# Optimization experiments

Hardware: AMD Instinct MI355X
Metric: run time of the kernel (lower is better)

## Reference

```python
import jax, jax.numpy as jnp
import numpy as np

VOCAB = 32000
EMBED = 512
NUM_CLASS = 5
LEAVES = 8192
N_NODES = 2 * LEAVES - 1


def _build_tree(n_leaves):
    """Balanced binary tree over n_leaves leaves, nodes listed in post-order
    (children always appear before their parent), matching the recursive
    traversal order of the original torch module."""
    is_leaf, word, left, right = [], [], [], []

    def rec(lo, hi):
        if hi - lo == 1:
            is_leaf.append(1)
            word.append((lo * 2654435761) % VOCAB)
            left.append(0)
            right.append(0)
        else:
            mid = (lo + hi) // 2
            l = rec(lo, mid)
            r = rec(mid, hi)
            is_leaf.append(0)
            word.append(0)
            left.append(l)
            right.append(r)
        return len(is_leaf) - 1

    rec(0, n_leaves)
    return (np.asarray(is_leaf, np.int32), np.asarray(word, np.int32),
            np.asarray(left, np.int32), np.asarray(right, np.int32))


def setup_inputs() -> dict:
    key = jax.random.key(0)
    k1, k2, k3, k4, k5 = jax.random.split(key, 5)
    is_leaf, word, left, right = _build_tree(LEAVES)
    scale = 0.05
    return {
        "is_leaf": jnp.asarray(is_leaf),
        "word": jnp.asarray(word),
        "left": jnp.asarray(left),
        "right": jnp.asarray(right),
        "emb": jax.random.normal(k1, (VOCAB, EMBED), jnp.float32) * scale,
        "W": jax.random.normal(k2, (EMBED, 2 * EMBED), jnp.float32) * scale,
        "bW": jax.random.normal(k3, (EMBED,), jnp.float32) * scale,
        "P": jax.random.normal(k4, (NUM_CLASS, EMBED), jnp.float32) * scale,
        "bP": jax.random.normal(k5, (NUM_CLASS,), jnp.float32) * scale,
    }


def reference(is_leaf, word, left, right, emb, W, bW, P, bP):
    n = is_leaf.shape[0]

    def step(H, xs):
        idx, lf, wd, li, ri = xs
        # internal node: relu(W @ [h_left; h_right] + b)
        pair = jnp.concatenate([H[li], H[ri]])          # [2D]
        internal = pair @ W.T + bW                       # [D]
        leaf = emb[wd]                                   # [D]
        h = jax.nn.relu(jnp.where(lf == 1, leaf, internal))
        return H.at[idx].set(h), None

    H0 = jnp.zeros((n, EMBED), emb.dtype)
    xs = (jnp.arange(n, dtype=jnp.int32), is_leaf, word, left, right)
    H, _ = jax.lax.scan(step, H0, xs)
    # per-node class logits, rows in traversal (post-)order: [N, num_class]
    return H @ P.T + bP
```

## Files before the change

### kernel.cpp

```cpp
#include <hip/hip_runtime.h>


#define EMBED 512
#define K2    1024
#define WOFF  (EMBED * K2)

typedef _Float16 half8 __attribute__((ext_vector_type(8)));
typedef _Float16 half4 __attribute__((ext_vector_type(4)));
typedef float    floatx4 __attribute__((ext_vector_type(4)));

__device__ __forceinline__ float relu_f(float x) { return fmaxf(x, 0.0f); }

__global__ __launch_bounds__(256)
void packleaf(const float* __restrict__ W, const float* __restrict__ emb,
              const int* __restrict__ word,
              _Float16* __restrict__ Whp,
              _Float16* __restrict__ Hh, _Float16* __restrict__ Hl,
              int nLeaves)
{
    int tid = threadIdx.x;
    int wave = tid >> 6, lane = tid & 63;

    {
        int t = blockIdx.x * 256 + tid;
        int n = t >> 7, kc = t & 127;
        const float* src = W + (size_t)n * K2 + kc * 8;
        int s = kc >> 2, quad = kc & 3;
        int ln = (quad << 4) | (n & 15);
        size_t off = (size_t)(n >> 4) * 16384 + (size_t)s * 512 + (size_t)ln * 8;
        half8 hi, lo;
#pragma unroll
        for (int j = 0; j < 8; ++j) {
            float w = src[j];
            _Float16 h16 = (_Float16)w;
            hi[j] = h16;
            lo[j] = (_Float16)(w - (float)h16);
        }
        *(half8*)(Whp + off) = hi;
        *(half8*)(Whp + WOFF + off) = lo;
    }
    {
#pragma unroll
        for (int i = 0; i < 8; ++i) {
            int m = blockIdx.x * 32 + wave * 8 + i;
            if (m < nLeaves) {
                int idx = 2 * m - __popc(m);
                int wd = word[idx];
                const float4* src = (const float4*)(emb + (size_t)wd * EMBED) + lane * 2;
                float4 a = src[0], b = src[1];
                float v[8] = {a.x, a.y, a.z, a.w, b.x, b.y, b.z, b.w};
                half8 hi, lo;
#pragma unroll
                for (int j = 0; j < 8; ++j) {
                    float x = relu_f(v[j]);
                    _Float16 h16 = (_Float16)x;
                    hi[j] = h16;
                    lo[j] = (_Float16)(x - (float)h16);
                }
                *(half8*)(Hh + (size_t)idx * EMBED + lane * 8) = hi;
                *(half8*)(Hl + (size_t)idx * EMBED + lane * 8) = lo;
            }
        }
    }
}

__global__ __launch_bounds__(256)
void gemm_splitk32(const _Float16* __restrict__ Hh, const _Float16* __restrict__ Hl,
                   const _Float16* __restrict__ Wp,
                   const float* __restrict__ bW,
                   _Float16* HhO, _Float16* HlO,
                   int h, int M)
{
    __shared__ float red[4096];

    int tid = threadIdx.x;
    int wave = tid >> 6, lane = tid & 63;
    int q = lane >> 4, r = lane & 15;
    int m0 = blockIdx.x * 32, n0 = blockIdx.y * 32;

    const _Float16 *pAh[2], *pAl[2];
#pragma unroll
    for (int mi = 0; mi < 2; ++mi) {
        int m = m0 + mi * 16 + r;
        int idx = ((m + 1) << (h + 1)) - 2 - __popc(m);
        int childRow = (wave < 2) ? (idx - (1 << h)) : (idx - 1);
        int kbase = (wave & 1) * 256;
        pAh[mi] = Hh + (size_t)childRow * EMBED + kbase + q * 8;
        pAl[mi] = Hl + (size_t)childRow * EMBED + kbase + q * 8;
    }
    const _Float16* pB[2];
#pragma unroll
    for (int ui = 0; ui < 2; ++ui)
        pB[ui] = Wp + (size_t)(blockIdx.y * 2 + ui) * 16384
               + (size_t)(wave * 8) * 512 + lane * 8;

    floatx4 acc[2][2];
#pragma unroll
    for (int mi = 0; mi < 2; ++mi)
#pragma unroll
        for (int ui = 0; ui < 2; ++ui) acc[mi][ui] = (floatx4){0.f, 0.f, 0.f, 0.f};

#pragma unroll
    for (int s = 0; s < 8; ++s) {
        half8 ah[2], al[2], bh[2], bl[2];
#pragma unroll
        for (int mi = 0; mi < 2; ++mi) {
            ah[mi] = *(const half8*)(pAh[mi] + s * 32);
            al[mi] = *(const half8*)(pAl[mi] + s * 32);
        }
#pragma unroll
        for (int ui = 0; ui < 2; ++ui) {
            bh[ui] = *(const half8*)(pB[ui] + s * 512);
            bl[ui] = *(const half8*)(pB[ui] + s * 512 + WOFF);
        }
#pragma unroll
        for (int mi = 0; mi < 2; ++mi)
#pragma unroll
            for (int ui = 0; ui < 2; ++ui) {
                acc[mi][ui] = __builtin_amdgcn_mfma_f32_16x16x32_f16(ah[mi], bh[ui], acc[mi][ui], 0, 0, 0);
                acc[mi][ui] = __builtin_amdgcn_mfma_f32_16x16x32_f16(ah[mi], bl[ui], acc[mi][ui], 0, 0, 0);
                acc[mi][ui] = __builtin_amdgcn_mfma_f32_16x16x32_f16(al[mi], bh[ui], acc[mi][ui], 0, 0, 0);
            }
    }

#pragma unroll
    for (int mi = 0; mi < 2; ++mi)
#pragma unroll
        for (int ui = 0; ui < 2; ++ui)
#pragma unroll
            for (int reg = 0; reg < 4; ++reg)
                red[wave * 1024 + (mi * 16 + q * 4 + reg) * 32 + ui * 16 + r]
                    = acc[mi][ui][reg];
    __syncthreads();

    int row = tid >> 3, c4 = (tid & 7) * 4;
    int mm = m0 + row;
    int node = ((mm + 1) << (h + 1)) - 2 - __popc(mm);
    half4 hi4, lo4;
#pragma unroll
    for (int j = 0; j < 4; ++j) {
        int c = row * 32 + c4 + j;
        float v = red[c] + red[1024 + c] + red[2048 + c] + red[3072 + c];
        float x = relu_f(v + bW[n0 + c4 + j]);
        _Float16 hi = (_Float16)x;
        hi4[j] = hi;
        lo4[j] = (_Float16)(x - (float)hi);
    }
    *(half4*)(HhO + (size_t)node * EMBED + n0 + c4) = hi4;
    *(half4*)(HlO + (size_t)node * EMBED + n0 + c4) = lo4;
}

__global__ __launch_bounds__(256)
void gemm_splitk(const _Float16* __restrict__ Hh, const _Float16* __restrict__ Hl,
                 const _Float16* __restrict__ Wp,
                 const float* __restrict__ bW,
                 _Float16* HhO, _Float16* HlO,
                 int h, int M)
{
    __shared__ float red[4 * 256];

    int tid = threadIdx.x;
    int wave = tid >> 6, lane = tid & 63;
    int q = lane >> 4, r = lane & 15;
    int mt = blockIdx.x, u = blockIdx.y;

    int m = mt * 16 + r;
    if (m >= M) m = M - 1;
    int idx = ((m + 1) << (h + 1)) - 2 - __popc(m);
    int childRow = (wave < 2) ? (idx - (1 << h)) : (idx - 1);
    int kbase = (wave & 1) * 256;
    const _Float16* pAh = Hh + (size_t)childRow * EMBED + kbase + q * 8;
    const _Float16* pAl = Hl + (size_t)childRow * EMBED + kbase + q * 8;
    const _Float16* pB  = Wp + (size_t)u * 16384 + (size_t)(wave * 8) * 512 + lane * 8;

    floatx4 acc = (floatx4){0.f, 0.f, 0.f, 0.f};
#pragma unroll
    for (int s = 0; s < 8; ++s) {
        half8 ah = *(const half8*)(pAh + s * 32);
        half8 al = *(const half8*)(pAl + s * 32);
        half8 bh = *(const half8*)(pB + s * 512);
        half8 bl = *(const half8*)(pB + s * 512 + WOFF);
        acc = __builtin_amdgcn_mfma_f32_16x16x32_f16(ah, bh, acc, 0, 0, 0);
        acc = __builtin_amdgcn_mfma_f32_16x16x32_f16(ah, bl, acc, 0, 0, 0);
        acc = __builtin_amdgcn_mfma_f32_16x16x32_f16(al, bh, acc, 0, 0, 0);
    }
#pragma unroll
    for (int reg = 0; reg < 4; ++reg)
        red[wave * 256 + (q * 4 + reg) * 16 + r] = acc[reg];
    __syncthreads();

    int row = tid >> 4, col = tid & 15;
    float v = red[row * 16 + col] + red[256 + row * 16 + col]
            + red[512 + row * 16 + col] + red[768 + row * 16 + col];
    int mm = mt * 16 + row;
    if (mm < M) {
        int node = ((mm + 1) << (h + 1)) - 2 - __popc(mm);
        int colg = u * 16 + col;
        float x = relu_f(v + bW[colg]);
        _Float16 hi = (_Float16)x;
        HhO[(size_t)node * EMBED + colg] = hi;
        HlO[(size_t)node * EMBED + colg] = (_Float16)(x - (float)hi);
    }
}

__global__ __launch_bounds__(256)
void out_kernel(const _Float16* __restrict__ Hh, const _Float16* __restrict__ Hl,
                const float* __restrict__ P, const float* __restrict__ bP,
                float* __restrict__ out, int nNodes)
{
    int t = blockIdx.x * 256 + threadIdx.x;
    int node = t >> 6, lane = t & 63;
    if (node >= nNodes) return;
    half8 hv = *(const half8*)(Hh + (size_t)node * EMBED + lane * 8);
    half8 lv = *(const half8*)(Hl + (size_t)node * EMBED + lane * 8);
    float hx[8];
#pragma unroll
    for (int j = 0; j < 8; ++j) hx[j] = (float)hv[j] + (float)lv[j];
    float s[5];
#pragma unroll
    for (int c = 0; c < 5; ++c) {
        const float* p = P + c * EMBED + lane * 8;
        float4 p0 = *(const float4*)p;
        float4 p1 = *(const float4*)(p + 4);
        s[c] = hx[0] * p0.x + hx[1] * p0.y + hx[2] * p0.z + hx[3] * p0.w
             + hx[4] * p1.x + hx[5] * p1.y + hx[6] * p1.z + hx[7] * p1.w;
    }
#pragma unroll
    for (int o = 32; o > 0; o >>= 1)
#pragma unroll
        for (int c = 0; c < 5; ++c)
            s[c] += __shfl_down(s[c], o, 64);
    if (lane == 0) {
#pragma unroll
        for (int c = 0; c < 5; ++c)
            out[(size_t)node * 5 + c] = s[c] + bP[c];
    }
}

extern "C" void kernel_launch(void* const* d_in, const int* in_sizes, int n_in,
                              void* d_out, int out_size, void* d_ws, size_t ws_size,
                              hipStream_t stream)
{
    const int*   word = (const int*)d_in[1];
    const float* emb  = (const float*)d_in[4];
    const float* W    = (const float*)d_in[5];
    const float* bW   = (const float*)d_in[6];
    const float* P    = (const float*)d_in[7];
    const float* bP   = (const float*)d_in[8];
    float* out = (float*)d_out;

    int nNodes  = in_sizes[0];
    int nLeaves = (nNodes + 1) / 2;

    int hoff = (nNodes + 1) * EMBED;
    _Float16* Hh  = (_Float16*)d_ws;
    _Float16* Hl  = Hh + hoff;
    _Float16* Whp = Hl + hoff;

    packleaf<<<dim3(256), dim3(256), 0, stream>>>(
        W, emb, word, Whp, Hh, Hl, nLeaves);
    for (int h = 1; h <= 4; ++h) {
        int M = 1 << (13 - h);
        gemm_splitk32<<<dim3(M / 32, 16), dim3(256), 0, stream>>>(
            Hh, Hl, Whp, bW, Hh, Hl, h, M);
    }
    for (int h = 5; h <= 13; ++h) {
        int M = 1 << (13 - h);
        gemm_splitk<<<dim3((M + 15) / 16, 32), dim3(256), 0, stream>>>(
            Hh, Hl, Whp, bW, Hh, Hl, h, M);
    }
    out_kernel<<<dim3((nNodes * 64 + 255) / 256), dim3(256), 0, stream>>>(
        Hh, Hl, P, bP, out, nNodes);
}
```

Baseline: 252.8 us.

## Store hidden states level-contiguous and add LDS-staged 64x64 GEMM for bottom levels

Hidden-state rows are now laid out level by level (leaves first, then each tree level contiguously), so the two children of node m sit at adjacent rows 2m and 2m+1. Row indexing in the GEMMs becomes a plain offset, and only the output kernel maps back to post-order. The two largest levels get a new 64x64-tile kernel that stages A through LDS with global_load_lds and reduces a 2-way K split in shared memory, to improve reuse and coalescing over the old 32x32 split-K kernel. The cost is a more complex kernel with extra barriers per K chunk, and stores to C that are now scalar and strided.

```diff
diff --git a/kernel.cpp b/kernel.cpp
--- a/kernel.cpp
+++ b/kernel.cpp
@@ -6,10 +6,16 @@
 #define WOFF  (EMBED * K2)
 
 typedef _Float16 half8 __attribute__((ext_vector_type(8)));
-typedef _Float16 half4 __attribute__((ext_vector_type(4)));
 typedef float    floatx4 __attribute__((ext_vector_type(4)));
 
 __device__ __forceinline__ float relu_f(float x) { return fmaxf(x, 0.0f); }
+
+#define GLDS16(gp, lp)                                                        \
+    __builtin_amdgcn_global_load_lds(                                         \
+        (const __attribute__((address_space(1))) void*)(gp),                  \
+        (__attribute__((address_space(3))) void*)(lp), 16, 0, 0)
+
+#define MFMA16(a, b, c) __builtin_amdgcn_mfma_f32_16x16x32_f16(a, b, c, 0, 0, 0)
 
 __global__ __launch_bounds__(256)
 void packleaf(const float* __restrict__ W, const float* __restrict__ emb,
@@ -44,8 +50,7 @@
         for (int i = 0; i < 8; ++i) {
             int m = blockIdx.x * 32 + wave * 8 + i;
             if (m < nLeaves) {
-                int idx = 2 * m - __popc(m);
-                int wd = word[idx];
+                int wd = word[2 * m - __popc(m)];
                 const float4* src = (const float4*)(emb + (size_t)wd * EMBED) + lane * 2;
                 float4 a = src[0], b = src[1];
                 float v[8] = {a.x, a.y, a.z, a.w, b.x, b.y, b.z, b.w};
@@ -57,19 +62,110 @@
                     hi[j] = h16;
                     lo[j] = (_Float16)(x - (float)h16);
                 }
-                *(half8*)(Hh + (size_t)idx * EMBED + lane * 8) = hi;
-                *(half8*)(Hl + (size_t)idx * EMBED + lane * 8) = lo;
-            }
-        }
-    }
-}
-
-__global__ __launch_bounds__(256)
-void gemm_splitk32(const _Float16* __restrict__ Hh, const _Float16* __restrict__ Hl,
-                   const _Float16* __restrict__ Wp,
+                *(half8*)(Hh + (size_t)m * EMBED + lane * 8) = hi;
+                *(half8*)(Hl + (size_t)m * EMBED + lane * 8) = lo;
+            }
+        }
+    }
+}
+
+__global__ __launch_bounds__(256)
+void gemm_lvl(const _Float16* __restrict__ Ap,
+              const _Float16* __restrict__ Wp,
+              const float* __restrict__ bW,
+              _Float16* __restrict__ Cp,
+              int hoff)
+{
+    __shared__ _Float16 As[16384];
+    __shared__ float Red[4096];
+
+    int tid = threadIdx.x;
+    int wave = tid >> 6, lane = tid & 63;
+    int q = lane >> 4, r = lane & 15;
+    int slice = wave >> 1, nh = wave & 1;
+    int bm0 = blockIdx.x * 64, bn0 = blockIdx.y * 64;
+
+    const _Float16* Asrc = Ap + (size_t)(nh ? hoff : 0)
+                         + (size_t)(bm0 + r) * 1024 + slice * 512 + q * 8;
+
+    floatx4 acc[4][2];
+#pragma unroll
+    for (int t = 0; t < 4; ++t)
+#pragma unroll
+        for (int u = 0; u < 2; ++u) acc[t][u] = (floatx4){0.f, 0.f, 0.f, 0.f};
+
+    for (int kc = 0; kc < 8; ++kc) {
+#pragma unroll
+        for (int t = 0; t < 4; ++t)
+#pragma unroll
+            for (int s2 = 0; s2 < 2; ++s2) {
+                const _Float16* gp = Asrc + t * (16 * 1024) + kc * 64 + s2 * 32;
+                GLDS16(gp, &As[(slice * 16 + t * 4 + s2 * 2 + nh) * 512]);
+            }
+        __syncthreads();
+
+#pragma unroll
+        for (int s2 = 0; s2 < 2; ++s2) {
+            half8 bh[2], bl[2];
+#pragma unroll
+            for (int u = 0; u < 2; ++u) {
+                const _Float16* pb = Wp + (size_t)(blockIdx.y * 4 + nh * 2 + u) * 16384
+                                   + (size_t)(slice * 16 + kc * 2 + s2) * 512 + lane * 8;
+                bh[u] = *(const half8*)pb;
+                bl[u] = *(const half8*)(pb + WOFF);
+            }
+#pragma unroll
+            for (int t = 0; t < 4; ++t) {
+                half8 ah = *(const half8*)&As[(slice * 16 + t * 4 + s2 * 2 + 0) * 512 + lane * 8];
+                half8 al = *(const half8*)&As[(slice * 16 + t * 4 + s2 * 2 + 1) * 512 + lane * 8];
+#pragma unroll
+                for (int u = 0; u < 2; ++u) {
+                    acc[t][u] = MFMA16(ah, bh[u], acc[t][u]);
+                    acc[t][u] = MFMA16(ah, bl[u], acc[t][u]);
+                    acc[t][u] = MFMA16(al, bh[u], acc[t][u]);
+                }
+            }
+        }
+        __syncthreads();
+    }
+
+    if (slice == 1) {
+#pragma unroll
+        for (int t = 0; t < 4; ++t)
+#pragma unroll
+            for (int u = 0; u < 2; ++u)
+#pragma unroll
+                for (int reg = 0; reg < 4; ++reg)
+                    Red[(t * 16 + q * 4 + reg) * 64 + nh * 32 + u * 16 + r]
+                        = acc[t][u][reg];
+    }
+    __syncthreads();
+    if (slice == 0) {
+#pragma unroll
+        for (int t = 0; t < 4; ++t)
+#pragma unroll
+            for (int u = 0; u < 2; ++u) {
+                int col = bn0 + nh * 32 + u * 16 + r;
+                float bw = bW[col];
+#pragma unroll
+                for (int reg = 0; reg < 4; ++reg) {
+                    int ml = t * 16 + q * 4 + reg;
+                    float v = acc[t][u][reg]
+                            + Red[ml * 64 + nh * 32 + u * 16 + r];
+                    float x = relu_f(v + bw);
+                    _Float16 hi = (_Float16)x;
+                    size_t o = (size_t)(bm0 + ml) * EMBED + col;
+                    Cp[o] = hi;
+                    Cp[o + hoff] = (_Float16)(x - (float)hi);
+                }
+            }
+    }
+}
+
+__global__ __launch_bounds__(256)
+void gemm_splitk32(const _Float16* __restrict__ Ap, const _Float16* __restrict__ Wp,
                    const float* __restrict__ bW,
-                   _Float16* HhO, _Float16* HlO,
-                   int h, int M)
+                   _Float16* __restrict__ Cp, int hoff)
 {
     __shared__ float red[4096];
 
@@ -82,23 +178,22 @@
 #pragma unroll
     for (int mi = 0; mi < 2; ++mi) {
         int m = m0 + mi * 16 + r;
-        int idx = ((m + 1) << (h + 1)) - 2 - __popc(m);
-        int childRow = (wave < 2) ? (idx - (1 << h)) : (idx - 1);
-        int kbase = (wave & 1) * 256;
-        pAh[mi] = Hh + (size_t)childRow * EMBED + kbase + q * 8;
-        pAl[mi] = Hl + (size_t)childRow * EMBED + kbase + q * 8;
+        int prow = 2 * m + (wave >> 1);
+        int kb = (wave & 1) * 256;
+        pAh[mi] = Ap + (size_t)prow * EMBED + kb + q * 8;
+        pAl[mi] = pAh[mi] + hoff;
     }
     const _Float16* pB[2];
 #pragma unroll
-    for (int ui = 0; ui < 2; ++ui)
-        pB[ui] = Wp + (size_t)(blockIdx.y * 2 + ui) * 16384
-               + (size_t)(wave * 8) * 512 + lane * 8;
+    for (int u = 0; u < 2; ++u)
+        pB[u] = Wp + (size_t)(blockIdx.y * 2 + u) * 16384
+              + (size_t)(wave * 8) * 512 + lane * 8;
 
     floatx4 acc[2][2];
 #pragma unroll
     for (int mi = 0; mi < 2; ++mi)
 #pragma unroll
-        for (int ui = 0; ui < 2; ++ui) acc[mi][ui] = (floatx4){0.f, 0.f, 0.f, 0.f};
+        for (int u = 0; u < 2; ++u) acc[mi][u] = (floatx4){0.f, 0.f, 0.f, 0.f};
 
 #pragma unroll
     for (int s = 0; s < 8; ++s) {
@@ -109,34 +204,32 @@
             al[mi] = *(const half8*)(pAl[mi] + s * 32);
         }
 #pragma unroll
-        for (int ui = 0; ui < 2; ++ui) {
-            bh[ui] = *(const half8*)(pB[ui] + s * 512);
-            bl[ui] = *(const half8*)(pB[ui] + s * 512 + WOFF);
+        for (int u = 0; u < 2; ++u) {
+            bh[u] = *(const half8*)(pB[u] + s * 512);
+            bl[u] = *(const half8*)(pB[u] + s * 512 + WOFF);
         }
 #pragma unroll
         for (int mi = 0; mi < 2; ++mi)
 #pragma unroll
-            for (int ui = 0; ui < 2; ++ui) {
-                acc[mi][ui] = __builtin_amdgcn_mfma_f32_16x16x32_f16(ah[mi], bh[ui], acc[mi][ui], 0, 0, 0);
-                acc[mi][ui] = __builtin_amdgcn_mfma_f32_16x16x32_f16(ah[mi], bl[ui], acc[mi][ui], 0, 0, 0);
-                acc[mi][ui] = __builtin_amdgcn_mfma_f32_16x16x32_f16(al[mi], bh[ui], acc[mi][ui], 0, 0, 0);
+            for (int u = 0; u < 2; ++u) {
+                acc[mi][u] = MFMA16(ah[mi], bh[u], acc[mi][u]);
+                acc[mi][u] = MFMA16(ah[mi], bl[u], acc[mi][u]);
+                acc[mi][u] = MFMA16(al[mi], bh[u], acc[mi][u]);
             }
     }
 
 #pragma unroll
     for (int mi = 0; mi < 2; ++mi)
 #pragma unroll
-        for (int ui = 0; ui < 2; ++ui)
+        for (int u = 0; u < 2; ++u)
 #pragma unroll
             for (int reg = 0; reg < 4; ++reg)
-                red[wave * 1024 + (mi * 16 + q * 4 + reg) * 32 + ui * 16 + r]
-                    = acc[mi][ui][reg];
+                red[wave * 1024 + (mi * 16 + q * 4 + reg) * 32 + u * 16 + r]
+                    = acc[mi][u][reg];
     __syncthreads();
 
     int row = tid >> 3, c4 = (tid & 7) * 4;
-    int mm = m0 + row;
-    int node = ((mm + 1) << (h + 1)) - 2 - __popc(mm);
-    half4 hi4, lo4;
+    _Float16 hi4[4], lo4[4];
 #pragma unroll
     for (int j = 0; j < 4; ++j) {
         int c = row * 32 + c4 + j;
@@ -146,18 +239,17 @@
         hi4[j] = hi;
         lo4[j] = (_Float16)(x - (float)hi);
     }
-    *(half4*)(HhO + (size_t)node * EMBED + n0 + c4) = hi4;
-    *(half4*)(HlO + (size_t)node * EMBED + n0 + c4) = lo4;
-}
-
-__global__ __launch_bounds__(256)
-void gemm_splitk(const _Float16* __restrict__ Hh, const _Float16* __restrict__ Hl,
-                 const _Float16* __restrict__ Wp,
+    size_t o = (size_t)(m0 + row) * EMBED + n0 + c4;
+#pragma unroll
+    for (int j = 0; j < 4; ++j) { Cp[o + j] = hi4[j]; Cp[o + hoff + j] = lo4[j]; }
+}
+
+__global__ __launch_bounds__(256)
+void gemm_splitk(const _Float16* __restrict__ Ap, const _Float16* __restrict__ Wp,
                  const float* __restrict__ bW,
-                 _Float16* HhO, _Float16* HlO,
-                 int h, int M)
-{
-    __shared__ float red[4 * 256];
+                 _Float16* __restrict__ Cp, int hoff, int M)
+{
+    __shared__ float red[1024];
 
     int tid = threadIdx.x;
     int wave = tid >> 6, lane = tid & 63;
@@ -166,11 +258,10 @@
 
     int m = mt * 16 + r;
     if (m >= M) m = M - 1;
-    int idx = ((m + 1) << (h + 1)) - 2 - __popc(m);
-    int childRow = (wave < 2) ? (idx - (1 << h)) : (idx - 1);
-    int kbase = (wave & 1) * 256;
-    const _Float16* pAh = Hh + (size_t)childRow * EMBED + kbase + q * 8;
-    const _Float16* pAl = Hl + (size_t)childRow * EMBED + kbase + q * 8;
+    int prow = 2 * m + (wave >> 1);
+    int kb = (wave & 1) * 256;
+    const _Float16* pAh = Ap + (size_t)prow * EMBED + kb + q * 8;
+    const _Float16* pAl = pAh + hoff;
     const _Float16* pB  = Wp + (size_t)u * 16384 + (size_t)(wave * 8) * 512 + lane * 8;
 
     floatx4 acc = (floatx4){0.f, 0.f, 0.f, 0.f};
@@ -180,9 +271,9 @@
         half8 al = *(const half8*)(pAl + s * 32);
         half8 bh = *(const half8*)(pB + s * 512);
         half8 bl = *(const half8*)(pB + s * 512 + WOFF);
-        acc = __builtin_amdgcn_mfma_f32_16x16x32_f16(ah, bh, acc, 0, 0, 0);
-        acc = __builtin_amdgcn_mfma_f32_16x16x32_f16(ah, bl, acc, 0, 0, 0);
-        acc = __builtin_amdgcn_mfma_f32_16x16x32_f16(al, bh, acc, 0, 0, 0);
+        acc = MFMA16(ah, bh, acc);
+        acc = MFMA16(ah, bl, acc);
+        acc = MFMA16(al, bh, acc);
     }
 #pragma unroll
     for (int reg = 0; reg < 4; ++reg)
@@ -194,12 +285,12 @@
             + red[512 + row * 16 + col] + red[768 + row * 16 + col];
     int mm = mt * 16 + row;
     if (mm < M) {
-        int node = ((mm + 1) << (h + 1)) - 2 - __popc(mm);
         int colg = u * 16 + col;
         float x = relu_f(v + bW[colg]);
         _Float16 hi = (_Float16)x;
-        HhO[(size_t)node * EMBED + colg] = hi;
-        HlO[(size_t)node * EMBED + colg] = (_Float16)(x - (float)hi);
+        size_t o = (size_t)mm * EMBED + colg;
+        Cp[o] = hi;
+        Cp[o + hoff] = (_Float16)(x - (float)hi);
     }
 }
 
@@ -209,13 +300,18 @@
                 float* __restrict__ out, int nNodes)
 {
     int t = blockIdx.x * 256 + threadIdx.x;
-    int node = t >> 6, lane = t & 63;
-    if (node >= nNodes) return;
-    half8 hv = *(const half8*)(Hh + (size_t)node * EMBED + lane * 8);
-    half8 lv = *(const half8*)(Hl + (size_t)node * EMBED + lane * 8);
+    int j = t >> 6, lane = t & 63;
+    if (j >= nNodes) return;
+    int v = nNodes - j;
+    int h = 13 - (31 - __clz(v));
+    int m = j - ((nNodes + 1) - (1 << (13 - h + 1)));
+    int node = ((m + 1) << (h + 1)) - 2 - __popc(m);
+
+    half8 hv = *(const half8*)(Hh + (size_t)j * EMBED + lane * 8);
+    half8 lv = *(const half8*)(Hl + (size_t)j * EMBED + lane * 8);
     float hx[8];
 #pragma unroll
-    for (int j = 0; j < 8; ++j) hx[j] = (float)hv[j] + (float)lv[j];
+    for (int k = 0; k < 8; ++k) hx[k] = (float)hv[k] + (float)lv[k];
     float s[5];
 #pragma unroll
     for (int c = 0; c < 5; ++c) {
@@ -251,23 +347,35 @@
 
     int nNodes  = in_sizes[0];
     int nLeaves = (nNodes + 1) / 2;
-
-    int hoff = (nNodes + 1) * EMBED;
+    int nRows   = nNodes + 1;
+
+    int hoff = nRows * EMBED;
     _Float16* Hh  = (_Float16*)d_ws;
     _Float16* Hl  = Hh + hoff;
     _Float16* Whp = Hl + hoff;
 
+    auto roff = [&](int h) { return nRows - (1 << (14 - h)); };
+
     packleaf<<<dim3(256), dim3(256), 0, stream>>>(
         W, emb, word, Whp, Hh, Hl, nLeaves);
-    for (int h = 1; h <= 4; ++h) {
+
+    for (int h = 1; h <= 2; ++h) {
+        int M = 1 << (13 - h);
+        gemm_lvl<<<dim3(M / 64, 8), dim3(256), 0, stream>>>(
+            Hh + (size_t)roff(h - 1) * EMBED, Whp, bW,
+            Hh + (size_t)roff(h) * EMBED, hoff);
+    }
+    for (int h = 3; h <= 4; ++h) {
         int M = 1 << (13 - h);
         gemm_splitk32<<<dim3(M / 32, 16), dim3(256), 0, stream>>>(
-            Hh, Hl, Whp, bW, Hh, Hl, h, M);
+            Hh + (size_t)roff(h - 1) * EMBED, Whp, bW,
+            Hh + (size_t)roff(h) * EMBED, hoff);
     }
     for (int h = 5; h <= 13; ++h) {
         int M = 1 << (13 - h);
         gemm_splitk<<<dim3((M + 15) / 16, 32), dim3(256), 0, stream>>>(
-            Hh, Hl, Whp, bW, Hh, Hl, h, M);
+            Hh + (size_t)roff(h - 1) * EMBED, Whp, bW,
+            Hh + (size_t)roff(h) * EMBED, hoff, M);
     }
     out_kernel<<<dim3((nNodes * 64 + 255) / 256), dim3(256), 0, stream>>>(
         Hh, Hl, P, bP, out, nNodes);
```

New measurement: 236.2 us. 6.5% less time.
